# Performance work log

Measured on AMD Instinct MI355X. Metric: run time of the kernel, lower is better.

Reference implementation:

```python
import jax, jax.numpy as jnp
import numpy as np

VOCAB = 50257
EMBED_DIM = 128
B = 32
T = 8192
MAX_LINES = 64


def setup_inputs() -> dict:
    key = jax.random.key(0)
    k1, k2, k3 = jax.random.split(key, 3)
    paragraph_variable = jax.random.randint(k1, (B, T), 0, VOCAB, dtype=jnp.int64)
    # sorted per-row segment ids encode the ragged sentence boundaries
    segment_ids = jnp.sort(jax.random.randint(k2, (B, T), 0, MAX_LINES, dtype=jnp.int64), axis=-1)
    embedding_table = jax.random.normal(k3, (VOCAB, EMBED_DIM), dtype=jnp.float32)
    return {
        "paragraph_variable": paragraph_variable,
        "segment_ids": segment_ids,
        "max_no_lines": MAX_LINES,
        "embedding_table": embedding_table,
    }


def reference(paragraph_variable, segment_ids, max_no_lines, embedding_table):
    b, t = paragraph_variable.shape
    d = embedding_table.shape[1]
    # embedding gather: [B, T, D]
    emb = embedding_table[paragraph_variable]
    # flatten batch into segment space: global segment id = b * max_no_lines + seg
    flat_seg = (jnp.arange(b, dtype=segment_ids.dtype)[:, None] * max_no_lines + segment_ids).reshape(-1)
    line_embedding = jax.ops.segment_sum(
        emb.reshape(b * t, d), flat_seg, num_segments=b * max_no_lines
    ).reshape(b, max_no_lines, d)
    return line_embedding
```

## Files before the change

kernel.cpp:

```cpp
#include <hip/hip_runtime.h>


#define D 128
#define MAXL 64

__device__ __forceinline__ int lower_bound_i32(const int* __restrict__ s, int n, int v) {
    int lo = 0, hi = n;
    while (lo < hi) {
        int mid = (lo + hi) >> 1;
        if (s[mid] < v) lo = mid + 1; else hi = mid;
    }
    return lo;
}

__global__ __launch_bounds__(256, 8) void seg_embed_sum_kernel(
    const int* __restrict__ tokens,
    const int* __restrict__ segs,
    const float* __restrict__ table,
    float* __restrict__ out,
    int T) {
    const int seg   = blockIdx.x;
    const int b     = blockIdx.y;
    const int tid   = threadIdx.x;
    const int group = tid >> 5;
    const int lane  = tid & 31;

    const int* srow = segs + (size_t)b * T;
    const int start = lower_bound_i32(srow, T, seg);
    const int end   = lower_bound_i32(srow, T, seg + 1);
    const int count = end - start;

    const int* trow = tokens + (size_t)b * T + start;

    const int per    = (count + 7) >> 3;
    const int gstart = group * per;
    const int gend   = min(count, gstart + per);

    float4 acc = make_float4(0.f, 0.f, 0.f, 0.f);

    for (int base = gstart; base < gend; base += 32) {
        const int n = min(32, gend - base);
        int tok = 0;
        if (lane < n) tok = trow[base + lane];
        #pragma unroll 4
        for (int j = 0; j < n; ++j) {
            const int t = __shfl(tok, j, 32);
            const float4 v = *reinterpret_cast<const float4*>(
                table + (size_t)t * D + lane * 4);
            acc.x += v.x; acc.y += v.y; acc.z += v.z; acc.w += v.w;
        }
    }

    __shared__ float red[8][D];
    *reinterpret_cast<float4*>(&red[group][lane * 4]) = acc;
    __syncthreads();

    if (tid < 32) {
        float4 s = make_float4(0.f, 0.f, 0.f, 0.f);
        #pragma unroll
        for (int g = 0; g < 8; ++g) {
            const float4 v = *reinterpret_cast<const float4*>(&red[g][tid * 4]);
            s.x += v.x; s.y += v.y; s.z += v.z; s.w += v.w;
        }
        *reinterpret_cast<float4*>(out + ((size_t)b * MAXL + seg) * D + tid * 4) = s;
    }
}

extern "C" void kernel_launch(void* const* d_in, const int* in_sizes, int n_in,
                              void* d_out, int out_size, void* d_ws, size_t ws_size,
                              hipStream_t stream) {
    const int* tokens  = (const int*)d_in[0];
    const int* segs    = (const int*)d_in[1];
    const float* table = (const float*)d_in[3];
    float* out         = (float*)d_out;

    const int B = out_size / (MAXL * D);
    const int T = in_sizes[0] / B;

    dim3 grid(MAXL, B);
    seg_embed_sum_kernel<<<grid, 256, 0, stream>>>(tokens, segs, table, out, T);
}
```

Measured before the change: 92.43 us.

## Use wave-parallel ballot search for segment bounds and unroll gather with dual accumulators

Replaces the serial per-thread binary search over 8192 segment ids with a two-level wave-wide search: ballot over strided samples, then a refinement pass. The block shares the resulting bounds through shared memory. The gather loop is also manually unrolled by four with two accumulators so more independent table loads are in flight. The fast search is specialized to T=8192 and falls back to the serial search otherwise, and it adds a block-wide barrier.

```diff
diff --git a/kernel.cpp b/kernel.cpp
--- a/kernel.cpp
+++ b/kernel.cpp
@@ -4,13 +4,28 @@
 #define D 128
 #define MAXL 64
 
-__device__ __forceinline__ int lower_bound_i32(const int* __restrict__ s, int n, int v) {
+__device__ __forceinline__ int lower_bound_serial(const int* __restrict__ s, int n, int v) {
     int lo = 0, hi = n;
     while (lo < hi) {
         int mid = (lo + hi) >> 1;
         if (s[mid] < v) lo = mid + 1; else hi = mid;
     }
     return lo;
+}
+
+__device__ __forceinline__ int wave_lower_bound_8192(const int* __restrict__ s, int v, int lane) {
+    int x1 = s[lane << 7];
+    unsigned long long m1 = __ballot(x1 < v);
+    int c1 = __popcll(m1);
+    if (c1 == 0) return 0;
+    const int lo = ((c1 - 1) << 7) + 1;
+    int x2 = s[lo + (lane << 1)];
+    unsigned long long m2 = __ballot(x2 < v);
+    int c2 = __popcll(m2);
+    if (c2 == 64) return lo + 127;
+    if (c2 == 0)  return lo;
+    const int a = lo + (c2 << 1) - 1;
+    return (s[a] < v) ? a + 1 : a;
 }
 
 __global__ __launch_bounds__(256, 8) void seg_embed_sum_kernel(
@@ -26,8 +41,20 @@
     const int lane  = tid & 31;
 
     const int* srow = segs + (size_t)b * T;
-    const int start = lower_bound_i32(srow, T, seg);
-    const int end   = lower_bound_i32(srow, T, seg + 1);
+
+    __shared__ int sbounds[2];
+    if (T == 8192) {
+        const int wave = tid >> 6;
+        const int wl   = tid & 63;
+        const int lb = wave_lower_bound_8192(srow, seg + (wave & 1), wl);
+        if (wl == 0) sbounds[wave & 1] = lb;
+    } else {
+        if (tid < 2) sbounds[tid] = lower_bound_serial(srow, T, seg + tid);
+    }
+    __syncthreads();
+
+    const int start = sbounds[0];
+    const int end   = sbounds[1];
     const int count = end - start;
 
     const int* trow = tokens + (size_t)b * T + start;
@@ -36,23 +63,38 @@
     const int gstart = group * per;
     const int gend   = min(count, gstart + per);
 
-    float4 acc = make_float4(0.f, 0.f, 0.f, 0.f);
+    float4 acc0 = make_float4(0.f, 0.f, 0.f, 0.f);
+    float4 acc1 = make_float4(0.f, 0.f, 0.f, 0.f);
 
     for (int base = gstart; base < gend; base += 32) {
         const int n = min(32, gend - base);
         int tok = 0;
         if (lane < n) tok = trow[base + lane];
-        #pragma unroll 4
-        for (int j = 0; j < n; ++j) {
+        int j = 0;
+        for (; j + 4 <= n; j += 4) {
+            const int t0 = __shfl(tok, j,     32);
+            const int t1 = __shfl(tok, j + 1, 32);
+            const int t2 = __shfl(tok, j + 2, 32);
+            const int t3 = __shfl(tok, j + 3, 32);
+            const float4 v0 = *reinterpret_cast<const float4*>(table + (size_t)t0 * D + lane * 4);
+            const float4 v1 = *reinterpret_cast<const float4*>(table + (size_t)t1 * D + lane * 4);
+            const float4 v2 = *reinterpret_cast<const float4*>(table + (size_t)t2 * D + lane * 4);
+            const float4 v3 = *reinterpret_cast<const float4*>(table + (size_t)t3 * D + lane * 4);
+            acc0.x += v0.x; acc0.y += v0.y; acc0.z += v0.z; acc0.w += v0.w;
+            acc1.x += v1.x; acc1.y += v1.y; acc1.z += v1.z; acc1.w += v1.w;
+            acc0.x += v2.x; acc0.y += v2.y; acc0.z += v2.z; acc0.w += v2.w;
+            acc1.x += v3.x; acc1.y += v3.y; acc1.z += v3.z; acc1.w += v3.w;
+        }
+        for (; j < n; ++j) {
             const int t = __shfl(tok, j, 32);
-            const float4 v = *reinterpret_cast<const float4*>(
-                table + (size_t)t * D + lane * 4);
-            acc.x += v.x; acc.y += v.y; acc.z += v.z; acc.w += v.w;
+            const float4 v = *reinterpret_cast<const float4*>(table + (size_t)t * D + lane * 4);
+            acc0.x += v.x; acc0.y += v.y; acc0.z += v.z; acc0.w += v.w;
         }
     }
+    acc0.x += acc1.x; acc0.y += acc1.y; acc0.z += acc1.z; acc0.w += acc1.w;
 
     __shared__ float red[8][D];
-    *reinterpret_cast<float4*>(&red[group][lane * 4]) = acc;
+    *reinterpret_cast<float4*>(&red[group][lane * 4]) = acc0;
     __syncthreads();
 
     if (tid < 32) {
```

Measured after the change: 89.47 us. 1.03x faster.
